# Kernel optimization log

Measured on AMD Instinct MI355X. Metric: run time of the kernel, lower is better.

The kernel has to match this reference:

```python
import jax, jax.numpy as jnp
import numpy as np

B, T, S, H, V, E = 32, 256, 32, 512, 128, 512


def setup_inputs() -> dict:
    key = jax.random.key(0)
    ks = jax.random.split(key, 20)
    f = lambda i, shape: jax.random.normal(ks[i], shape, jnp.float32) * 0.05
    return dict(
        embedding=f(0, (V, H)),
        scope_enc=f(1, (B, S, H)),
        spec_enc=f(2, (B, E)),
        W_init=f(3, (H, E)), b_init=jnp.zeros((H,), jnp.float32),
        W_ih=f(4, (3 * H, 2 * H)), W_hh=f(5, (3 * H, H)),
        b_ih=jnp.zeros((3 * H,), jnp.float32), b_hh=jnp.zeros((3 * H,), jnp.float32),
        W_out=f(6, (V, H)), b_out=jnp.zeros((V,), jnp.float32),
        Wd=f(7, (H, H)), We=f(8, (H, H)), v_attn=f(9, (H,)),
        tokens_in=jax.random.randint(ks[10], (B, T), 0, V),
        tokens_out=jax.random.randint(ks[11], (B, T), 0, V),
        pointer_ids=jax.random.randint(ks[12], (B, T), 0, S),
        ptr_targets=jax.random.randint(ks[13], (B, T), 0, S),
        pointer_mask=jax.random.bernoulli(ks[14], 0.25, (B, T)),
    )


def _gru(x_proj, h0, W_hh, b_hh):
    # x_proj: [B,T,3H] precomputed input projection; torch GRU gate order (r,z,n)
    def step(h, xp):
        gh = h @ W_hh.T + b_hh
        xr, xz, xn = jnp.split(xp, 3, axis=-1)
        hr, hz, hn = jnp.split(gh, 3, axis=-1)
        r = jax.nn.sigmoid(xr + hr)
        z = jax.nn.sigmoid(xz + hz)
        n = jnp.tanh(xn + r * hn)
        h_new = (1.0 - z) * n + z * h
        return h_new, h_new
    _, outs = jax.lax.scan(step, h0, jnp.swapaxes(x_proj, 0, 1))
    return jnp.swapaxes(outs, 0, 1)  # [B,T,H]


def reference(embedding, scope_enc, spec_enc, W_init, b_init, W_ih, W_hh, b_ih, b_hh,
              W_out, b_out, Wd, We, v_attn,
              tokens_in, tokens_out, pointer_ids, ptr_targets, pointer_mask):
    h0 = spec_enc @ W_init.T + b_init                      # initialState
    x_emb = embedding[tokens_in]                           # [B,T,H]
    obj = jax.vmap(lambda s, i: s[i])(scope_enc, pointer_ids)  # [B,T,H]
    obj = jnp.where(pointer_mask[:, :, None], obj, 0.0)    # objectInputs (zeros for non-pointers)
    x = jnp.concatenate([x_emb, obj], axis=-1)             # [B,T,2H]
    x_proj = x @ W_ih.T + b_ih                             # [B,T,3H]
    o = _gru(x_proj, h0, W_hh, b_hh)                       # decoder states [B,T,H]

    # token log-likelihood: -nll_loss(log_softmax(output(o)), targets), summed
    logp = jax.nn.log_softmax(o @ W_out.T + b_out, axis=-1)
    tok_ll = jnp.take_along_axis(logp, tokens_out[:, :, None], axis=-1)[..., 0].sum(-1)

    # pointer attention: additive attention with tanh, log_softmax over scope
    hd = o @ Wd.T                                          # decoderToPointer [B,T,H]
    ok = scope_enc @ We.T                                  # encoderToPointer [B,S,H]
    att = jnp.tanh(hd[:, :, None, :] + ok[:, None, :, :]) @ v_attn  # [B,T,S]
    logatt = jax.nn.log_softmax(att, axis=-1)
    ptr_ll = jnp.take_along_axis(logatt, ptr_targets[:, :, None], axis=-1)[..., 0]
    ptr_ll = jnp.where(pointer_mask, ptr_ll, 0.0).sum(-1)

    return tok_ll + ptr_ll  # per-program likelihood [B]
```

## Files before the change

kernel.cpp:

```cpp
#include <hip/hip_runtime.h>
#include <stdint.h>

#define NB 32
#define NT 256
#define NS 32
#define NH 512
#define NV 128
#define BT 8192

typedef __attribute__((ext_vector_type(8))) __bf16 bf16x8;
typedef __attribute__((ext_vector_type(4))) float f32x4;
typedef __attribute__((ext_vector_type(2))) _Float16 half2v;
typedef unsigned long long u64;

typedef __attribute__((address_space(1))) const unsigned int GASU;
typedef __attribute__((address_space(3))) unsigned int LASU;
#define ASYNC16(g, l) __builtin_amdgcn_global_load_lds((GASU*)(g), (LASU*)(l), 16, 0, 0)

__device__ __forceinline__ half2v pkrtz(float a, float b){
  return __builtin_bit_cast(half2v, __builtin_amdgcn_cvt_pkrtz(a, b));
}
__device__ __forceinline__ unsigned short f2bf(float f){
  unsigned int u = __builtin_bit_cast(unsigned int, f);
  u += 0x7fffu + ((u >> 16) & 1u);
  return (unsigned short)(u >> 16);
}
__device__ __forceinline__ float bf2f(unsigned short h){
  return __builtin_bit_cast(float, ((unsigned int)h) << 16);
}
__device__ __forceinline__ float fexp(float x){ return __builtin_amdgcn_exp2f(x * 1.4426950408889634f); }
__device__ __forceinline__ float fsigm(float x){ return __builtin_amdgcn_rcpf(1.f + fexp(-x)); }
__device__ __forceinline__ float ftanh(float x){
  float t = __builtin_amdgcn_exp2f(x * 2.8853900817779268f);
  return (t - 1.f) * __builtin_amdgcn_rcpf(t + 1.f);
}
__device__ __forceinline__ float flog(float x){ return __builtin_amdgcn_logf(x) * 0.6931471805599453f; }

__device__ __forceinline__ void st_l2(u64* p, u64 v){
  asm volatile("global_store_dwordx2 %0, %1, off" :: "v"(p), "v"(v) : "memory");
}

#define BAR() do{ \
  asm volatile("s_waitcnt lgkmcnt(0)" ::: "memory"); \
  __builtin_amdgcn_sched_barrier(0); \
  __builtin_amdgcn_s_barrier(); \
  __builtin_amdgcn_sched_barrier(0); \
}while(0)

__global__ void k_prep(const float* __restrict__ emb, const float* __restrict__ scope,
                       const float* __restrict__ Wih, const float* __restrict__ Wout,
                       const float* __restrict__ Wd,  const float* __restrict__ We,
                       unsigned short* e_o, unsigned short* s_o, unsigned short* wi_o,
                       unsigned short* wo_o, unsigned short* wd_o, unsigned short* we_o,
                       u64* hx, u64* hxL, float* out){
  int g = blockIdx.x*256 + threadIdx.x, gs = gridDim.x*256;
  if (g < 2*NB*256){
    hx[g] = 0ull;
    __hip_atomic_store(hxL + g, 0ull, __ATOMIC_RELAXED, __HIP_MEMORY_SCOPE_AGENT);
  }
  if (g < NB) out[g] = 0.f;
  for (int i=g; i<NV*NH;      i+=gs) e_o[i]  = f2bf(emb[i]);
  for (int i=g; i<NB*NS*NH;   i+=gs) s_o[i]  = f2bf(scope[i]);
  for (int i=g; i<3*NH*2*NH;  i+=gs) wi_o[i] = f2bf(Wih[i]);
  for (int i=g; i<NV*NH;      i+=gs) wo_o[i] = f2bf(Wout[i]);
  for (int i=g; i<NH*NH;      i+=gs) wd_o[i] = f2bf(Wd[i]);
  for (int i=g; i<NH*NH;      i+=gs) we_o[i] = f2bf(We[i]);
}

__global__ void k_h0(const float* __restrict__ spec, const float* __restrict__ Winit,
                     const float* __restrict__ binit, float* __restrict__ h032,
                     u64* __restrict__ hx, u64* __restrict__ hxL){
  const int b = blockIdx.x, tid = threadIdx.x, lane = tid & 63, w = tid >> 6;
  __shared__ float sp[NH];
  __shared__ float hres[NH];
  if (tid < 128) *(float4*)&sp[tid*4] = *(const float4*)(spec + b*NH + tid*4);
  __syncthreads();
  for (int i = 0; i < 128; ++i){
    int j = w * 128 + i;
    const float4* wr = (const float4*)(Winit + (size_t)j * NH);
    float4 x0 = wr[lane*2], x1 = wr[lane*2 + 1];
    float p = x0.x*sp[lane*8]   + x0.y*sp[lane*8+1] + x0.z*sp[lane*8+2] + x0.w*sp[lane*8+3]
            + x1.x*sp[lane*8+4] + x1.y*sp[lane*8+5] + x1.z*sp[lane*8+6] + x1.w*sp[lane*8+7];
    #pragma unroll
    for (int o = 1; o < 64; o <<= 1) p += __shfl_xor(p, o);
    if (lane == 0){
      float v = p + binit[j];
      h032[b*NH + j] = v;
      hres[j] = v;
    }
  }
  __syncthreads();
  if (tid < 256){
    unsigned int pw = __builtin_bit_cast(unsigned int, pkrtz(hres[2*tid], hres[2*tid+1]));
    u64 pv = (1ull << 32) | (u64)pw;
    __hip_atomic_store(hx + b*256 + tid, pv, __ATOMIC_RELAXED, __HIP_MEMORY_SCOPE_AGENT);
    __hip_atomic_store(hxL + b*256 + tid, pv, __ATOMIC_RELAXED, __HIP_MEMORY_SCOPE_AGENT);
  }
}

__global__ __launch_bounds__(256, 2) void k_gemm(
    const unsigned short* __restrict__ A, const unsigned short* __restrict__ Bw,
    float* __restrict__ Cf, unsigned short* __restrict__ Cbf,
    const float* __restrict__ bias, int M, int N, int K, int ldb)
{
  __shared__ unsigned short lA[2][128][64];
  __shared__ unsigned short lB[2][128][64];
  const int tid = threadIdx.x, lane = tid & 63, wv = tid >> 6;
  const int m0 = blockIdx.x * 128, n0 = blockIdx.y * 128;

  const unsigned short* srcA[4];
  const unsigned short* srcB[4];
  #pragma unroll
  for (int i = 0; i < 4; ++i){
    int ar = m0 + wv*32 + i*8 + (lane >> 3);
    int chunk = (lane & 7) * 8;
    srcA[i] = A + (size_t)ar * K + chunk;
    int br = n0 + wv*32 + i*8 + (lane >> 3);
    srcB[i] = Bw + (size_t)br * ldb + chunk;
  }

  f32x4 acc[4][4];
  #pragma unroll
  for (int x=0;x<4;++x)
    #pragma unroll
    for (int y=0;y<4;++y) acc[x][y] = (f32x4){0.f,0.f,0.f,0.f};

  auto STAGE = [&](int bf, int kt){
    const int k0 = kt * 64;
    #pragma unroll
    for (int i = 0; i < 4; ++i){
      ASYNC16(srcA[i] + k0, &lA[bf][wv*32 + i*8][0]);
      ASYNC16(srcB[i] + k0, &lB[bf][wv*32 + i*8][0]);
    }
  };

  STAGE(0, 0);
  asm volatile("s_waitcnt vmcnt(0)" ::: "memory");
  __syncthreads();

  const int wm = (wv >> 1) * 64, wn = (wv & 1) * 64;
  const int fr = lane & 15, fq = lane >> 4;
  const int nt = K >> 6;
  int cur = 0;
  for (int kt = 0; kt < nt; ++kt){
    if (kt + 1 < nt) STAGE(cur ^ 1, kt + 1);
    #pragma unroll
    for (int ks = 0; ks < 2; ++ks){
      bf16x8 af[4], bfv[4];
      #pragma unroll
      for (int mi = 0; mi < 4; ++mi)
        af[mi] = *(const bf16x8*)&lA[cur][wm + mi*16 + fr][ks*32 + fq*8];
      #pragma unroll
      for (int ni = 0; ni < 4; ++ni)
        bfv[ni] = *(const bf16x8*)&lB[cur][wn + ni*16 + fr][ks*32 + fq*8];
      #pragma unroll
      for (int mi = 0; mi < 4; ++mi)
        #pragma unroll
        for (int ni = 0; ni < 4; ++ni)
          acc[mi][ni] = __builtin_amdgcn_mfma_f32_16x16x32_bf16(af[mi], bfv[ni], acc[mi][ni], 0, 0, 0);
    }
    asm volatile("s_waitcnt vmcnt(0)" ::: "memory");
    __syncthreads();
    cur ^= 1;
  }

  #pragma unroll
  for (int mi = 0; mi < 4; ++mi){
    #pragma unroll
    for (int ni = 0; ni < 4; ++ni){
      int col = n0 + wn + ni*16 + fr;
      float bv = bias ? bias[col] : 0.f;
      #pragma unroll
      for (int rr = 0; rr < 4; ++rr){
        int row = m0 + wm + mi*16 + fq*4 + rr;
        float v = acc[mi][ni][rr] + bv;
        if (Cbf) Cbf[(size_t)row * N + col] = f2bf(v);
        else     Cf [(size_t)row * N + col] = v;
      }
    }
  }
}

__global__ __launch_bounds__(512, 1) void k_gru(
    const float* __restrict__ Whh, const float* __restrict__ bhh,
    const unsigned short* __restrict__ embp,
    const unsigned short* __restrict__ objp,
    const int* __restrict__ tokin, const int* __restrict__ pids,
    const int* __restrict__ pmask,
    const float* __restrict__ h032,
    u64* __restrict__ hx,
    u64* __restrict__ hxL,
    unsigned short* __restrict__ obf)
{
  const int bid = blockIdx.x;
  const int b = bid & 31, s = bid >> 5;
  const int tid = threadIdx.x;
  const int u = tid >> 3, r = tid & 7;
  const int jg = s * 64 + u;

  __shared__ __align__(16) unsigned int hl[256];
  __shared__ float xpl[192];
  __shared__ unsigned int pkb[32];

  half2v w0[8][4], w1[8][4], w2[8][4];
  #pragma unroll
  for (int c = 0; c < 8; ++c){
    const int kb = r*64 + ((c + r) & 7) * 8;
    const float* p0 = Whh + ((size_t)(       jg)) * NH + kb;
    const float* p1 = Whh + ((size_t)(  NH + jg)) * NH + kb;
    const float* p2 = Whh + ((size_t)(2*NH + jg)) * NH + kb;
    #pragma unroll
    for (int p = 0; p < 4; ++p){
      float2 a = *(const float2*)(p0 + 2*p);
      float2 c2 = *(const float2*)(p1 + 2*p);
      float2 d = *(const float2*)(p2 + 2*p);
      w0[c][p] = pkrtz(a.x, a.y);
      w1[c][p] = pkrtz(c2.x, c2.y);
      w2[c][p] = pkrtz(d.x, d.y);
    }
  }
  const float bh0 = bhh[jg], bh1 = bhh[NH + jg], bh2 = bhh[2*NH + jg];
  float hprev = h032[b*NH + jg];

  unsigned short xe = 0, xo = 0; int mk = 0;
  int jcol = 0;
  if (tid >= 256 && tid < 448){
    int idx = tid - 256;
    jcol = (idx >> 6) * NH + s*64 + (idx & 63);
    int tk = tokin[b*NT + 0];
    int pd = pids [b*NT + 0];
    mk     = pmask[b*NT + 0];
    xe = embp[(size_t)tk * 1536 + jcol];
    xo = objp[((size_t)(b*NS + pd)) * 1536 + jcol];
  }
  __syncthreads();

  for (int t = 0; t < NT; ++t){
    if (tid < 256){
      const int base = (((t & 1) * NB + b) << 8) + tid;
      const u64* pL = hxL + base;
      const u64* pM = hx + base;
      const unsigned int want = (unsigned int)(t + 1);
      u64 v;
      u64 a  = __hip_atomic_load(pL, __ATOMIC_RELAXED, __HIP_MEMORY_SCOPE_AGENT);
      u64 b2 = __hip_atomic_load(pL, __ATOMIC_RELAXED, __HIP_MEMORY_SCOPE_AGENT);
      int it = 0;
      while (true){
        if ((unsigned int)(a >> 32) == want){ v = a; break; }
        a = b2;
        b2 = __hip_atomic_load(pL, __ATOMIC_RELAXED, __HIP_MEMORY_SCOPE_AGENT);
        if (((++it) & 7) == 0){
          u64 m = __hip_atomic_load(pM, __ATOMIC_RELAXED, __HIP_MEMORY_SCOPE_AGENT);
          if ((unsigned int)(m >> 32) == want){ v = m; break; }
        }
      }
      hl[tid] = (unsigned int)v;
    } else if (tid < 448){
      int idx = tid - 256;
      xpl[idx] = bf2f(xe) + (mk ? bf2f(xo) : 0.f);
      if (t + 1 < NT){
        int tk = tokin[b*NT + t + 1];
        int pd = pids [b*NT + t + 1];
        mk     = pmask[b*NT + t + 1];
        xe = embp[(size_t)tk * 1536 + jcol];
        xo = objp[((size_t)(b*NS + pd)) * 1536 + jcol];
      }
    }
    BAR();

    float a0 = 0.f, a1 = 0.f, a2 = 0.f;
    half2v hch[8][4];
    #pragma unroll
    for (int c = 0; c < 8; ++c){
      const int g = (r << 3) + ((c + r) & 7);
      uint4 hv = *(const uint4*)&hl[g * 4];
      hch[c][0] = __builtin_bit_cast(half2v, hv.x);
      hch[c][1] = __builtin_bit_cast(half2v, hv.y);
      hch[c][2] = __builtin_bit_cast(half2v, hv.z);
      hch[c][3] = __builtin_bit_cast(half2v, hv.w);
    }
    #pragma unroll
    for (int c = 0; c < 8; ++c){
      #pragma unroll
      for (int p = 0; p < 4; ++p){
        a0 = __builtin_amdgcn_fdot2(w0[c][p], hch[c][p], a0, false);
        a1 = __builtin_amdgcn_fdot2(w1[c][p], hch[c][p], a1, false);
        a2 = __builtin_amdgcn_fdot2(w2[c][p], hch[c][p], a2, false);
      }
    }
    a0 += __shfl_xor(a0, 1); a0 += __shfl_xor(a0, 2); a0 += __shfl_xor(a0, 4);
    a1 += __shfl_xor(a1, 1); a1 += __shfl_xor(a1, 2); a1 += __shfl_xor(a1, 4);
    a2 += __shfl_xor(a2, 1); a2 += __shfl_xor(a2, 2); a2 += __shfl_xor(a2, 4);

    float hnew = 0.f;
    if (r == 0){
      float xr = xpl[u], xz = xpl[64 + u], xn = xpl[128 + u];
      float rg = fsigm(xr + a0 + bh0);
      float zg = fsigm(xz + a1 + bh1);
      float ng = ftanh(xn + rg * (a2 + bh2));
      hnew = (1.f - zg) * ng + zg * hprev;
      hprev = hnew;
    }
    float hpart = __shfl_xor(hnew, 8);
    if (r == 0 && (u & 1) == 0){
      unsigned int pw = __builtin_bit_cast(unsigned int, pkrtz(hnew, hpart));
      u64 pv = ((u64)(unsigned int)(t + 2) << 32) | (u64)pw;
      const int dst = ((((t + 1) & 1) * NB + b) << 8) + (s << 5) + (u >> 1);
      st_l2(hxL + dst, pv);
      __hip_atomic_store(hx + dst, pv,
                         __ATOMIC_RELAXED, __HIP_MEMORY_SCOPE_AGENT);
      pkb[u >> 1] = (unsigned int)f2bf(hnew) | ((unsigned int)f2bf(hpart) << 16);
    }
    BAR();

    if (tid >= 448 && tid < 480){
      int i = tid - 448;
      ((unsigned int*)obf)[((size_t)(b*NT + t)) * (NH/2) + s*32 + i] = pkb[i];
    }
  }
}

__global__ void k_tokll(const float* __restrict__ logits, const int* __restrict__ tko,
                        float* __restrict__ out){
  const int tid = threadIdx.x, lane = tid & 63, w = tid >> 6;
  const int r0 = blockIdx.x * 64 + w * 16;
  const int b = r0 >> 8;
  int mytok = 0; float tval = 0.f;
  if (lane < 16){
    mytok = tko[r0 + lane];
    tval = logits[(size_t)(r0 + lane) * NV + mytok];
  }
  float acc = 0.f;
  for (int i = 0; i < 16; ++i){
    const float* L = logits + (size_t)(r0 + i) * NV;
    float l0 = L[lane], l1 = L[64 + lane];
    float m = fmaxf(l0, l1);
    #pragma unroll
    for (int o = 1; o < 64; o <<= 1) m = fmaxf(m, __shfl_xor(m, o));
    float sm = fexp(l0 - m) + fexp(l1 - m);
    #pragma unroll
    for (int o = 1; o < 64; o <<= 1) sm += __shfl_xor(sm, o);
    float lse = m + flog(sm);
    float tv = __shfl(tval, i);
    if (lane == 0) acc += tv - lse;
  }
  if (lane == 0) atomicAdd(out + b, acc);
}

__global__ __launch_bounds__(256, 2) void k_ptr(
    const unsigned short* __restrict__ hd, const float* __restrict__ okp,
    const float* __restrict__ vat, const int* __restrict__ ptg,
    const int* __restrict__ pmask, float* __restrict__ out)
{
  __shared__ unsigned short okl[NS][518];
  __shared__ unsigned short hdl[16][518];
  __shared__ float vl[NH];
  __shared__ float attl[16][33];
  const int tid = threadIdx.x;
  const int b = blockIdx.x >> 4, t0 = (blockIdx.x & 15) * 16;
  for (int ii = 0; ii < 64; ++ii){
    int lin = ii*256 + tid;
    int s = lin >> 9, h = lin & 511;
    okl[s][h] = f2bf(okp[((size_t)(b*NS + s)) * NH + h]);
  }
  for (int ii = 0; ii < 32; ++ii){
    int lin = ii*256 + tid;
    int tt = lin >> 9, h = lin & 511;
    hdl[tt][h] = hd[((size_t)(b*NT + t0 + tt)) * NH + h];
  }
  vl[tid] = vat[tid]; vl[256 + tid] = vat[256 + tid];
  __syncthreads();
  #pragma unroll
  for (int pp = 0; pp < 2; ++pp){
    int p = pp*256 + tid;
    int tt = p >> 5, s = p & 31;
    float a = 0.f;
    #pragma unroll 4
    for (int h = 0; h < NH; ++h)
      a += vl[h] * ftanh(bf2f(hdl[tt][h]) + bf2f(okl[s][h]));
    attl[tt][s] = a;
  }
  __syncthreads();
  if (tid < 16){
    int tt = tid;
    float m = -1e30f;
    for (int s = 0; s < NS; ++s) m = fmaxf(m, attl[tt][s]);
    float sm = 0.f;
    for (int s = 0; s < NS; ++s) sm += fexp(attl[tt][s] - m);
    float lse = m + flog(sm);
    int g = b*NT + t0 + tt;
    float c = pmask[g] ? (attl[tt][ptg[g]] - lse) : 0.f;
    #pragma unroll
    for (int o = 1; o < 16; o <<= 1) c += __shfl_xor(c, o);
    if (tid == 0) atomicAdd(out + b, c);
  }
}

extern "C" void kernel_launch(void* const* d_in, const int* in_sizes, int n_in,
                              void* d_out, int out_size, void* d_ws, size_t ws_size,
                              hipStream_t stream)
{
  (void)in_sizes; (void)n_in; (void)out_size; (void)ws_size;
  const float* embedding  = (const float*)d_in[0];
  const float* scope_enc  = (const float*)d_in[1];
  const float* spec_enc   = (const float*)d_in[2];
  const float* W_init     = (const float*)d_in[3];
  const float* b_init     = (const float*)d_in[4];
  const float* W_ih       = (const float*)d_in[5];
  const float* W_hh       = (const float*)d_in[6];
  const float* b_ih       = (const float*)d_in[7];
  const float* b_hh       = (const float*)d_in[8];
  const float* W_out      = (const float*)d_in[9];
  const float* b_out      = (const float*)d_in[10];
  const float* Wd         = (const float*)d_in[11];
  const float* We         = (const float*)d_in[12];
  const float* v_attn     = (const float*)d_in[13];
  const int* tokens_in    = (const int*)d_in[14];
  const int* tokens_out   = (const int*)d_in[15];
  const int* pointer_ids  = (const int*)d_in[16];
  const int* ptr_targets  = (const int*)d_in[17];
  const int* pointer_mask = (const int*)d_in[18];
  float* outF = (float*)d_out;

  uint8_t* wp = (uint8_t*)d_ws;
  auto carve = [&](size_t bytes)->void*{
    void* p = (void*)wp; wp += (bytes + 255) & ~(size_t)255; return p;
  };
  unsigned short* embp_bf  = (unsigned short*)carve((size_t)NV*1536*2);
  unsigned short* objp_bf  = (unsigned short*)carve((size_t)NB*NS*1536*2);
  unsigned short* o_bf     = (unsigned short*)carve((size_t)BT*NH*2);
  float*          logitsF  = (float*)carve((size_t)BT*NV*4);
  unsigned short* hd_bf    = (unsigned short*)carve((size_t)BT*NH*2);
  float*          okp      = (float*)carve((size_t)NB*NS*NH*4);
  unsigned short* emb_bf   = (unsigned short*)carve((size_t)NV*NH*2);
  unsigned short* scope_bf = (unsigned short*)carve((size_t)NB*NS*NH*2);
  unsigned short* Wih_bf   = (unsigned short*)carve((size_t)3*NH*2*NH*2);
  unsigned short* Wout_bf  = (unsigned short*)carve((size_t)NV*NH*2);
  unsigned short* Wd_bf    = (unsigned short*)carve((size_t)NH*NH*2);
  unsigned short* We_bf    = (unsigned short*)carve((size_t)NH*NH*2);
  float*          h032     = (float*)carve((size_t)NB*NH*4);
  u64*            hx       = (u64*)carve((size_t)2*NB*256*8);
  u64*            hxL      = (u64*)carve((size_t)2*NB*256*8);

  hipLaunchKernelGGL(k_prep, dim3(1024), dim3(256), 0, stream,
                     embedding, scope_enc, W_ih, W_out, Wd, We,
                     emb_bf, scope_bf, Wih_bf, Wout_bf, Wd_bf, We_bf,
                     hx, hxL, outF);
  hipLaunchKernelGGL(k_h0, dim3(NB), dim3(256), 0, stream, spec_enc, W_init, b_init,
                     h032, hx, hxL);
  hipLaunchKernelGGL(k_gemm, dim3(1,12), dim3(256), 0, stream,
                     emb_bf, Wih_bf, (float*)nullptr, embp_bf,
                     b_ih, NV, 1536, NH, 1024);
  hipLaunchKernelGGL(k_gemm, dim3(8,12), dim3(256), 0, stream,
                     scope_bf, Wih_bf + NH, (float*)nullptr, objp_bf,
                     (const float*)nullptr, NB*NS, 1536, NH, 1024);
  hipLaunchKernelGGL(k_gru, dim3(256), dim3(512), 0, stream,
                     W_hh, b_hh, embp_bf, objp_bf, tokens_in, pointer_ids,
                     pointer_mask, h032, hx, hxL, o_bf);
  hipLaunchKernelGGL(k_gemm, dim3(64,1), dim3(256), 0, stream,
                     o_bf, Wout_bf, logitsF, (unsigned short*)nullptr, b_out,
                     BT, NV, NH, NH);
  hipLaunchKernelGGL(k_gemm, dim3(64,4), dim3(256), 0, stream,
                     o_bf, Wd_bf, (float*)nullptr, hd_bf, (const float*)nullptr,
                     BT, NH, NH, NH);
  hipLaunchKernelGGL(k_gemm, dim3(8,4), dim3(256), 0, stream,
                     scope_bf, We_bf, okp, (unsigned short*)nullptr,
                     (const float*)nullptr, NB*NS, NH, NH, NH);
  hipLaunchKernelGGL(k_tokll, dim3(128), dim3(256), 0, stream, logitsF, tokens_out, outF);
  hipLaunchKernelGGL(k_ptr, dim3(512), dim3(256), 0, stream,
                     hd_bf, okp, v_attn, ptr_targets, pointer_mask, outF);
}
```

Before: 596.6 us.

## Process two batch rows per GRU block and fuse output GEMM with token log-softmax

The persistent GRU kernel now handles two batch rows per block, halving the grid to 128 blocks. Each block reuses its register-resident W_hh slice for both rows and all 512 threads spin on the cross-block hidden-state exchange. The aim is fewer blocks in the per-step global synchronisation and more arithmetic per weight load, at the cost of double dot-product work per step on the serial critical path. Separately, the output-projection GEMM is fused with the log-softmax and target gather into one kernel, removing the fp32 logits buffer round trip and one launch.

```diff
diff --git a/kernel.cpp b/kernel.cpp
--- a/kernel.cpp
+++ b/kernel.cpp
@@ -181,6 +181,109 @@
   }
 }
 
+__global__ __launch_bounds__(256, 2) void k_logll(
+    const unsigned short* __restrict__ A, const unsigned short* __restrict__ Bw,
+    const float* __restrict__ bias, const int* __restrict__ tko,
+    float* __restrict__ out)
+{
+  __shared__ unsigned short lA[2][128][64];
+  __shared__ unsigned short lB[2][128][64];
+  __shared__ float pmax[128][2], psum[128][2], tgt[128], part[2];
+  const int tid = threadIdx.x, lane = tid & 63, wv = tid >> 6;
+  const int m0 = blockIdx.x * 128;
+
+  const unsigned short* srcA[4];
+  const unsigned short* srcB[4];
+  #pragma unroll
+  for (int i = 0; i < 4; ++i){
+    int ar = m0 + wv*32 + i*8 + (lane >> 3);
+    int chunk = (lane & 7) * 8;
+    srcA[i] = A + (size_t)ar * NH + chunk;
+    int br = wv*32 + i*8 + (lane >> 3);
+    srcB[i] = Bw + (size_t)br * NH + chunk;
+  }
+
+  f32x4 acc[4][4];
+  #pragma unroll
+  for (int x=0;x<4;++x)
+    #pragma unroll
+    for (int y=0;y<4;++y) acc[x][y] = (f32x4){0.f,0.f,0.f,0.f};
+
+  auto STAGE = [&](int bf, int kt){
+    const int k0 = kt * 64;
+    #pragma unroll
+    for (int i = 0; i < 4; ++i){
+      ASYNC16(srcA[i] + k0, &lA[bf][wv*32 + i*8][0]);
+      ASYNC16(srcB[i] + k0, &lB[bf][wv*32 + i*8][0]);
+    }
+  };
+
+  STAGE(0, 0);
+  asm volatile("s_waitcnt vmcnt(0)" ::: "memory");
+  __syncthreads();
+
+  const int wm = (wv >> 1) * 64, wn = (wv & 1) * 64;
+  const int fr = lane & 15, fq = lane >> 4;
+  int cur = 0;
+  for (int kt = 0; kt < 8; ++kt){
+    if (kt + 1 < 8) STAGE(cur ^ 1, kt + 1);
+    #pragma unroll
+    for (int ks = 0; ks < 2; ++ks){
+      bf16x8 af[4], bfv[4];
+      #pragma unroll
+      for (int mi = 0; mi < 4; ++mi)
+        af[mi] = *(const bf16x8*)&lA[cur][wm + mi*16 + fr][ks*32 + fq*8];
+      #pragma unroll
+      for (int ni = 0; ni < 4; ++ni)
+        bfv[ni] = *(const bf16x8*)&lB[cur][wn + ni*16 + fr][ks*32 + fq*8];
+      #pragma unroll
+      for (int mi = 0; mi < 4; ++mi)
+        #pragma unroll
+        for (int ni = 0; ni < 4; ++ni)
+          acc[mi][ni] = __builtin_amdgcn_mfma_f32_16x16x32_bf16(af[mi], bfv[ni], acc[mi][ni], 0, 0, 0);
+    }
+    asm volatile("s_waitcnt vmcnt(0)" ::: "memory");
+    __syncthreads();
+    cur ^= 1;
+  }
+
+  float bv[4];
+  #pragma unroll
+  for (int ni = 0; ni < 4; ++ni) bv[ni] = bias[wn + ni*16 + fr];
+  #pragma unroll
+  for (int mi = 0; mi < 4; ++mi){
+    #pragma unroll
+    for (int rr = 0; rr < 4; ++rr){
+      const int rowL = wm + mi*16 + fq*4 + rr;
+      float v[4];
+      #pragma unroll
+      for (int ni = 0; ni < 4; ++ni) v[ni] = acc[mi][ni][rr] + bv[ni];
+      int tk = tko[m0 + rowL];
+      int rel = tk - wn;
+      if (rel >= 0 && rel < 64 && fr == (rel & 15)) tgt[rowL] = v[rel >> 4];
+      float m = fmaxf(fmaxf(v[0], v[1]), fmaxf(v[2], v[3]));
+      #pragma unroll
+      for (int o = 1; o < 16; o <<= 1) m = fmaxf(m, __shfl_xor(m, o));
+      float sm = fexp(v[0]-m) + fexp(v[1]-m) + fexp(v[2]-m) + fexp(v[3]-m);
+      #pragma unroll
+      for (int o = 1; o < 16; o <<= 1) sm += __shfl_xor(sm, o);
+      if (fr == 0){ pmax[rowL][wv & 1] = m; psum[rowL][wv & 1] = sm; }
+    }
+  }
+  __syncthreads();
+  if (tid < 128){
+    float m0h = pmax[tid][0], m1h = pmax[tid][1];
+    float M = fmaxf(m0h, m1h);
+    float S = psum[tid][0]*fexp(m0h - M) + psum[tid][1]*fexp(m1h - M);
+    float ll = tgt[tid] - (M + flog(S));
+    #pragma unroll
+    for (int o = 1; o < 64; o <<= 1) ll += __shfl_xor(ll, o);
+    if ((tid & 63) == 0) part[tid >> 6] = ll;
+  }
+  __syncthreads();
+  if (tid == 0) atomicAdd(out + (m0 >> 8), part[0] + part[1]);
+}
+
 __global__ __launch_bounds__(512, 1) void k_gru(
     const float* __restrict__ Whh, const float* __restrict__ bhh,
     const unsigned short* __restrict__ embp,
@@ -188,19 +291,19 @@
     const int* __restrict__ tokin, const int* __restrict__ pids,
     const int* __restrict__ pmask,
     const float* __restrict__ h032,
-    u64* __restrict__ hx,
-    u64* __restrict__ hxL,
+    u64* __restrict__ hx, u64* __restrict__ hxL,
     unsigned short* __restrict__ obf)
 {
   const int bid = blockIdx.x;
-  const int b = bid & 31, s = bid >> 5;
+  const int pair = bid & 15, s = bid >> 4;
+  const int b0 = pair << 1, b1 = b0 | 1;
   const int tid = threadIdx.x;
   const int u = tid >> 3, r = tid & 7;
   const int jg = s * 64 + u;
 
-  __shared__ __align__(16) unsigned int hl[256];
-  __shared__ float xpl[192];
-  __shared__ unsigned int pkb[32];
+  __shared__ __align__(16) unsigned int hl[2][256];
+  __shared__ float xpl[2][192];
+  __shared__ unsigned int pkb[64];
 
   half2v w0[8][4], w1[8][4], w2[8][4];
   #pragma unroll
@@ -220,24 +323,39 @@
     }
   }
   const float bh0 = bhh[jg], bh1 = bhh[NH + jg], bh2 = bhh[2*NH + jg];
-  float hprev = h032[b*NH + jg];
-
-  unsigned short xe = 0, xo = 0; int mk = 0;
-  int jcol = 0;
-  if (tid >= 256 && tid < 448){
-    int idx = tid - 256;
-    jcol = (idx >> 6) * NH + s*64 + (idx & 63);
-    int tk = tokin[b*NT + 0];
-    int pd = pids [b*NT + 0];
-    mk     = pmask[b*NT + 0];
+  float hprev0 = h032[b0*NH + jg], hprev1 = h032[b1*NH + jg];
+
+  const int gb = (tid < 192) ? 0 : ((tid < 384) ? 1 : -1);
+  const int gslot = (gb == 0) ? tid : tid - 192;
+  int jcol = 0, mk = 0;
+  unsigned short xe = 0, xo = 0;
+  if (gb >= 0){
+    const int gbb = gb ? b1 : b0;
+    jcol = (gslot >> 6) * NH + s*64 + (gslot & 63);
+    int tk = tokin[gbb*NT + 0];
+    int pd = pids [gbb*NT + 0];
+    mk     = pmask[gbb*NT + 0];
     xe = embp[(size_t)tk * 1536 + jcol];
-    xo = objp[((size_t)(b*NS + pd)) * 1536 + jcol];
-  }
+    xo = objp[((size_t)(gbb*NS + pd)) * 1536 + jcol];
+  }
+  const int pb = tid >> 8, widx = tid & 255;
+  const int pbb = pb ? b1 : b0;
   __syncthreads();
 
   for (int t = 0; t < NT; ++t){
-    if (tid < 256){
-      const int base = (((t & 1) * NB + b) << 8) + tid;
+    if (gb >= 0){
+      const int gbb = gb ? b1 : b0;
+      xpl[gb][gslot] = bf2f(xe) + (mk ? bf2f(xo) : 0.f);
+      if (t + 1 < NT){
+        int tk = tokin[gbb*NT + t + 1];
+        int pd = pids [gbb*NT + t + 1];
+        mk     = pmask[gbb*NT + t + 1];
+        xe = embp[(size_t)tk * 1536 + jcol];
+        xo = objp[((size_t)(gbb*NS + pd)) * 1536 + jcol];
+      }
+    }
+    {
+      const int base = (((t & 1) * NB + pbb) << 8) + widx;
       const u64* pL = hxL + base;
       const u64* pM = hx + base;
       const unsigned int want = (unsigned int)(t + 1);
@@ -254,97 +372,95 @@
           if ((unsigned int)(m >> 32) == want){ v = m; break; }
         }
       }
-      hl[tid] = (unsigned int)v;
-    } else if (tid < 448){
-      int idx = tid - 256;
-      xpl[idx] = bf2f(xe) + (mk ? bf2f(xo) : 0.f);
-      if (t + 1 < NT){
-        int tk = tokin[b*NT + t + 1];
-        int pd = pids [b*NT + t + 1];
-        mk     = pmask[b*NT + t + 1];
-        xe = embp[(size_t)tk * 1536 + jcol];
-        xo = objp[((size_t)(b*NS + pd)) * 1536 + jcol];
-      }
+      hl[pb][widx] = (unsigned int)v;
     }
     BAR();
 
-    float a0 = 0.f, a1 = 0.f, a2 = 0.f;
-    half2v hch[8][4];
+    float a00=0.f, a01=0.f, a02=0.f, a10=0.f, a11=0.f, a12=0.f;
     #pragma unroll
     for (int c = 0; c < 8; ++c){
       const int g = (r << 3) + ((c + r) & 7);
-      uint4 hv = *(const uint4*)&hl[g * 4];
-      hch[c][0] = __builtin_bit_cast(half2v, hv.x);
-      hch[c][1] = __builtin_bit_cast(half2v, hv.y);
-      hch[c][2] = __builtin_bit_cast(half2v, hv.z);
-      hch[c][3] = __builtin_bit_cast(half2v, hv.w);
-    }
-    #pragma unroll
-    for (int c = 0; c < 8; ++c){
-      #pragma unroll
-      for (int p = 0; p < 4; ++p){
-        a0 = __builtin_amdgcn_fdot2(w0[c][p], hch[c][p], a0, false);
-        a1 = __builtin_amdgcn_fdot2(w1[c][p], hch[c][p], a1, false);
-        a2 = __builtin_amdgcn_fdot2(w2[c][p], hch[c][p], a2, false);
-      }
-    }
-    a0 += __shfl_xor(a0, 1); a0 += __shfl_xor(a0, 2); a0 += __shfl_xor(a0, 4);
-    a1 += __shfl_xor(a1, 1); a1 += __shfl_xor(a1, 2); a1 += __shfl_xor(a1, 4);
-    a2 += __shfl_xor(a2, 1); a2 += __shfl_xor(a2, 2); a2 += __shfl_xor(a2, 4);
-
-    float hnew = 0.f;
+      uint4 hv0 = *(const uint4*)&hl[0][g * 4];
+      uint4 hv1 = *(const uint4*)&hl[1][g * 4];
+      half2v h00 = __builtin_bit_cast(half2v, hv0.x);
+      half2v h01 = __builtin_bit_cast(half2v, hv0.y);
+      half2v h02 = __builtin_bit_cast(half2v, hv0.z);
+      half2v h03 = __builtin_bit_cast(half2v, hv0.w);
+      half2v h10 = __builtin_bit_cast(half2v, hv1.x);
+      half2v h11 = __builtin_bit_cast(half2v, hv1.y);
+      half2v h12 = __builtin_bit_cast(half2v, hv1.z);
+      half2v h13 = __builtin_bit_cast(half2v, hv1.w);
+      a00 = __builtin_amdgcn_fdot2(w0[c][0], h00, a00, false);
+      a00 = __builtin_amdgcn_fdot2(w0[c][1], h01, a00, false);
+      a00 = __builtin_amdgcn_fdot2(w0[c][2], h02, a00, false);
+      a00 = __builtin_amdgcn_fdot2(w0[c][3], h03, a00, false);
+      a01 = __builtin_amdgcn_fdot2(w1[c][0], h00, a01, false);
+      a01 = __builtin_amdgcn_fdot2(w1[c][1], h01, a01, false);
+      a01 = __builtin_amdgcn_fdot2(w1[c][2], h02, a01, false);
+      a01 = __builtin_amdgcn_fdot2(w1[c][3], h03, a01, false);
+      a02 = __builtin_amdgcn_fdot2(w2[c][0], h00, a02, false);
+      a02 = __builtin_amdgcn_fdot2(w2[c][1], h01, a02, false);
+      a02 = __builtin_amdgcn_fdot2(w2[c][2], h02, a02, false);
+      a02 = __builtin_amdgcn_fdot2(w2[c][3], h03, a02, false);
+      a10 = __builtin_amdgcn_fdot2(w0[c][0], h10, a10, false);
+      a10 = __builtin_amdgcn_fdot2(w0[c][1], h11, a10, false);
+      a10 = __builtin_amdgcn_fdot2(w0[c][2], h12, a10, false);
+      a10 = __builtin_amdgcn_fdot2(w0[c][3], h13, a10, false);
+      a11 = __builtin_amdgcn_fdot2(w1[c][0], h10, a11, false);
+      a11 = __builtin_amdgcn_fdot2(w1[c][1], h11, a11, false);
+      a11 = __builtin_amdgcn_fdot2(w1[c][2], h12, a11, false);
+      a11 = __builtin_amdgcn_fdot2(w1[c][3], h13, a11, false);
+      a12 = __builtin_amdgcn_fdot2(w2[c][0], h10, a12, false);
+      a12 = __builtin_amdgcn_fdot2(w2[c][1], h11, a12, false);
+      a12 = __builtin_amdgcn_fdot2(w2[c][2], h12, a12, false);
+      a12 = __builtin_amdgcn_fdot2(w2[c][3], h13, a12, false);
+    }
+    a00 += __shfl_xor(a00, 1); a00 += __shfl_xor(a00, 2); a00 += __shfl_xor(a00, 4);
+    a01 += __shfl_xor(a01, 1); a01 += __shfl_xor(a01, 2); a01 += __shfl_xor(a01, 4);
+    a02 += __shfl_xor(a02, 1); a02 += __shfl_xor(a02, 2); a02 += __shfl_xor(a02, 4);
+    a10 += __shfl_xor(a10, 1); a10 += __shfl_xor(a10, 2); a10 += __shfl_xor(a10, 4);
+    a11 += __shfl_xor(a11, 1); a11 += __shfl_xor(a11, 2); a11 += __shfl_xor(a11, 4);
+    a12 += __shfl_xor(a12, 1); a12 += __shfl_xor(a12, 2); a12 += __shfl_xor(a12, 4);
+
+    float hn0 = 0.f, hn1 = 0.f;
     if (r == 0){
-      float xr = xpl[u], xz = xpl[64 + u], xn = xpl[128 + u];
-      float rg = fsigm(xr + a0 + bh0);
-      float zg = fsigm(xz + a1 + bh1);
-      float ng = ftanh(xn + rg * (a2 + bh2));
-      hnew = (1.f - zg) * ng + zg * hprev;
-      hprev = hnew;
-    }
-    float hpart = __shfl_xor(hnew, 8);
+      float xr0 = xpl[0][u], xz0 = xpl[0][64 + u], xn0 = xpl[0][128 + u];
+      float rg0 = fsigm(xr0 + a00 + bh0);
+      float zg0 = fsigm(xz0 + a01 + bh1);
+      float ng0 = ftanh(xn0 + rg0 * (a02 + bh2));
+      hn0 = (1.f - zg0) * ng0 + zg0 * hprev0; hprev0 = hn0;
+      float xr1 = xpl[1][u], xz1 = xpl[1][64 + u], xn1 = xpl[1][128 + u];
+      float rg1 = fsigm(xr1 + a10 + bh0);
+      float zg1 = fsigm(xz1 + a11 + bh1);
+      float ng1 = ftanh(xn1 + rg1 * (a12 + bh2));
+      hn1 = (1.f - zg1) * ng1 + zg1 * hprev1; hprev1 = hn1;
+    }
+    float hp0 = __shfl_xor(hn0, 8);
+    float hp1 = __shfl_xor(hn1, 8);
     if (r == 0 && (u & 1) == 0){
-      unsigned int pw = __builtin_bit_cast(unsigned int, pkrtz(hnew, hpart));
-      u64 pv = ((u64)(unsigned int)(t + 2) << 32) | (u64)pw;
-      const int dst = ((((t + 1) & 1) * NB + b) << 8) + (s << 5) + (u >> 1);
-      st_l2(hxL + dst, pv);
-      __hip_atomic_store(hx + dst, pv,
-                         __ATOMIC_RELAXED, __HIP_MEMORY_SCOPE_AGENT);
-      pkb[u >> 1] = (unsigned int)f2bf(hnew) | ((unsigned int)f2bf(hpart) << 16);
+      const u64 tg = (u64)(unsigned int)(t + 2) << 32;
+      unsigned int pw0 = __builtin_bit_cast(unsigned int, pkrtz(hn0, hp0));
+      unsigned int pw1 = __builtin_bit_cast(unsigned int, pkrtz(hn1, hp1));
+      const int wofs = (s << 5) + (u >> 1);
+      const int pb0 = ((((t + 1) & 1) * NB + b0) << 8) + wofs;
+      const int pb1 = ((((t + 1) & 1) * NB + b1) << 8) + wofs;
+      u64 pv0 = tg | (u64)pw0, pv1 = tg | (u64)pw1;
+      st_l2(hxL + pb0, pv0);
+      st_l2(hxL + pb1, pv1);
+      __hip_atomic_store(hx + pb0, pv0, __ATOMIC_RELAXED, __HIP_MEMORY_SCOPE_AGENT);
+      __hip_atomic_store(hx + pb1, pv1, __ATOMIC_RELAXED, __HIP_MEMORY_SCOPE_AGENT);
+      pkb[(u >> 1)]      = (unsigned int)f2bf(hn0) | ((unsigned int)f2bf(hp0) << 16);
+      pkb[32 + (u >> 1)] = (unsigned int)f2bf(hn1) | ((unsigned int)f2bf(hp1) << 16);
     }
     BAR();
 
-    if (tid >= 448 && tid < 480){
+    if (tid >= 448){
       int i = tid - 448;
-      ((unsigned int*)obf)[((size_t)(b*NT + t)) * (NH/2) + s*32 + i] = pkb[i];
-    }
-  }
-}
-
-__global__ void k_tokll(const float* __restrict__ logits, const int* __restrict__ tko,
-                        float* __restrict__ out){
-  const int tid = threadIdx.x, lane = tid & 63, w = tid >> 6;
-  const int r0 = blockIdx.x * 64 + w * 16;
-  const int b = r0 >> 8;
-  int mytok = 0; float tval = 0.f;
-  if (lane < 16){
-    mytok = tko[r0 + lane];
-    tval = logits[(size_t)(r0 + lane) * NV + mytok];
-  }
-  float acc = 0.f;
-  for (int i = 0; i < 16; ++i){
-    const float* L = logits + (size_t)(r0 + i) * NV;
-    float l0 = L[lane], l1 = L[64 + lane];
-    float m = fmaxf(l0, l1);
-    #pragma unroll
-    for (int o = 1; o < 64; o <<= 1) m = fmaxf(m, __shfl_xor(m, o));
-    float sm = fexp(l0 - m) + fexp(l1 - m);
-    #pragma unroll
-    for (int o = 1; o < 64; o <<= 1) sm += __shfl_xor(sm, o);
-    float lse = m + flog(sm);
-    float tv = __shfl(tval, i);
-    if (lane == 0) acc += tv - lse;
-  }
-  if (lane == 0) atomicAdd(out + b, acc);
+      int bb = (i < 32) ? b0 : b1;
+      int ii = i & 31;
+      ((unsigned int*)obf)[((size_t)(bb*NT + t)) * (NH/2) + s*32 + ii] = pkb[i];
+    }
+  }
 }
 
 __global__ __launch_bounds__(256, 2) void k_ptr(
@@ -429,7 +545,6 @@
   unsigned short* embp_bf  = (unsigned short*)carve((size_t)NV*1536*2);
   unsigned short* objp_bf  = (unsigned short*)carve((size_t)NB*NS*1536*2);
   unsigned short* o_bf     = (unsigned short*)carve((size_t)BT*NH*2);
-  float*          logitsF  = (float*)carve((size_t)BT*NV*4);
   unsigned short* hd_bf    = (unsigned short*)carve((size_t)BT*NH*2);
   float*          okp      = (float*)carve((size_t)NB*NS*NH*4);
   unsigned short* emb_bf   = (unsigned short*)carve((size_t)NV*NH*2);
@@ -454,19 +569,17 @@
   hipLaunchKernelGGL(k_gemm, dim3(8,12), dim3(256), 0, stream,
                      scope_bf, Wih_bf + NH, (float*)nullptr, objp_bf,
                      (const float*)nullptr, NB*NS, 1536, NH, 1024);
-  hipLaunchKernelGGL(k_gru, dim3(256), dim3(512), 0, stream,
+  hipLaunchKernelGGL(k_gru, dim3(128), dim3(512), 0, stream,
                      W_hh, b_hh, embp_bf, objp_bf, tokens_in, pointer_ids,
                      pointer_mask, h032, hx, hxL, o_bf);
-  hipLaunchKernelGGL(k_gemm, dim3(64,1), dim3(256), 0, stream,
-                     o_bf, Wout_bf, logitsF, (unsigned short*)nullptr, b_out,
-                     BT, NV, NH, NH);
+  hipLaunchKernelGGL(k_logll, dim3(64), dim3(256), 0, stream,
+                     o_bf, Wout_bf, b_out, tokens_out, outF);
   hipLaunchKernelGGL(k_gemm, dim3(64,4), dim3(256), 0, stream,
                      o_bf, Wd_bf, (float*)nullptr, hd_bf, (const float*)nullptr,
                      BT, NH, NH, NH);
   hipLaunchKernelGGL(k_gemm, dim3(8,4), dim3(256), 0, stream,
                      scope_bf, We_bf, okp, (unsigned short*)nullptr,
                      (const float*)nullptr, NB*NS, NH, NH, NH);
-  hipLaunchKernelGGL(k_tokll, dim3(128), dim3(256), 0, stream, logitsF, tokens_out, outF);
   hipLaunchKernelGGL(k_ptr, dim3(512), dim3(256), 0, stream,
                      hd_bf, okp, v_attn, ptr_targets, pointer_mask, outF);
 }
```

After: 804.3 us. +34.8%, slower.
